# Kernel tuning notes

Hardware: AMD Instinct MI355X
Metric: run time of the kernel (lower is better)

The kernel has to match this reference:

```python
import jax, jax.numpy as jnp
import numpy as np

B, T, A, H, V = 2, 512, 768, 256, 70110  # batch, frames, audio_dim, gru_hidden, vertice_dim


def setup_inputs() -> dict:
    key = jax.random.key(0)
    ks = jax.random.split(key, 16)
    def p(k, shape, s=0.05):
        return jax.random.normal(k, shape, jnp.float32) * s
    return {
        "hidden_states": p(ks[0], (B, T, A), 1.0),
        "template": p(ks[1], (B, V), 1.0),
        "vertice": p(ks[2], (B, T, V), 1.0),
        "tf_mask": jax.random.randint(ks[3], (T,), 0, 2, jnp.int32),
        # GRU layer 0: input 2*A -> H ; layer 1: H -> H (PyTorch gate order r,z,n)
        "w_ih_l0": p(ks[4], (3 * H, 2 * A)),
        "w_hh_l0": p(ks[5], (3 * H, H)),
        "b_ih_l0": p(ks[6], (3 * H,)),
        "b_hh_l0": p(ks[7], (3 * H,)),
        "w_ih_l1": p(ks[8], (3 * H, H)),
        "w_hh_l1": p(ks[9], (3 * H, H)),
        "b_ih_l1": p(ks[10], (3 * H,)),
        "b_hh_l1": p(ks[11], (3 * H,)),
        "fc_w": p(ks[12], (V, H)),
        "fc_b": p(ks[13], (V,)),
        "red_w": p(ks[14], (A, V), 0.005),
        "red_b": p(ks[15], (A,)),
    }


def gru_cell(x, h, w_ih, w_hh, b_ih, b_hh):
    # PyTorch GRUCell math, gates ordered (r, z, n)
    gi = x @ w_ih.T + b_ih
    gh = h @ w_hh.T + b_hh
    i_r, i_z, i_n = jnp.split(gi, 3, axis=-1)
    h_r, h_z, h_n = jnp.split(gh, 3, axis=-1)
    r = jax.nn.sigmoid(i_r + h_r)
    z = jax.nn.sigmoid(i_z + h_z)
    n = jnp.tanh(i_n + r * h_n)
    return (1.0 - z) * n + z * h


def reference(hidden_states, template, vertice, tf_mask,
              w_ih_l0, w_hh_l0, b_ih_l0, b_hh_l0,
              w_ih_l1, w_hh_l1, b_ih_l1, b_hh_l1,
              fc_w, fc_b, red_w, red_b):
    dt = hidden_states.dtype
    cur = template @ red_w.T + red_b            # [B, A] reduced template vertice
    h_l0 = jnp.zeros((B, H), dt)
    h_l1 = jnp.zeros((B, H), dt)

    def step(carry, xs):
        h0, h1, cur = carry
        hs_t, vert_t, tf = xs                   # [B,A], [B,V], scalar int
        x = jnp.concatenate([hs_t, cur], axis=-1)   # [B, 2A]
        h0 = gru_cell(x, h0, w_ih_l0, w_hh_l0, b_ih_l0, b_hh_l0)
        h1 = gru_cell(h0, h1, w_ih_l1, w_hh_l1, b_ih_l1, b_hh_l1)
        pred = h1 @ fc_w.T + fc_b               # [B, V]
        loss_t = jnp.mean((pred - vert_t) ** 2)  # MSE criterion
        # teacher forcing: feed GT frame when tf==1, else own prediction
        src = jnp.where(tf.astype(bool), vert_t, pred)
        cur = src @ red_w.T + red_b             # [B, A]
        return (h0, h1, cur), (pred, loss_t)

    xs = (jnp.swapaxes(hidden_states, 0, 1),    # [T,B,A]
          jnp.swapaxes(vertice, 0, 1),          # [T,B,V]
          tf_mask)                              # [T]
    _, (preds, losses) = jax.lax.scan(step, (h_l0, h_l1, cur), xs)
    vertice_out = jnp.swapaxes(preds, 0, 1)     # [B,T,V]
    loss = jnp.mean(losses)                     # sum_t loss_t / frame_num
    return vertice_out, loss
```

## Files before the change

### kernel.cpp

```cpp
#include <hip/hip_runtime.h>
#include <hip/hip_bf16.h>


#define TT 512
#define VD 70110
#define NR 1024

using bf16x8 = __attribute__((ext_vector_type(8))) short;
using f32x4  = __attribute__((ext_vector_type(4))) float;

static __device__ __forceinline__ unsigned short f2bf(float f) {
  unsigned u = __float_as_uint(f);
  u += 0x7FFFu + ((u >> 16) & 1u);
  return (unsigned short)(u >> 16);
}

__global__ __launch_bounds__(512, 1)
void bigk_merged(const float* __restrict__ A, const float* __restrict__ vert,
                 const float* __restrict__ fcw,
                 float* __restrict__ OUTG, float* __restrict__ OUTM, int CHK)
{
  __shared__ unsigned short Al[256][40];
  __shared__ unsigned short Bl[256][40];
  const int tid = threadIdx.x;
  const bool bform = (blockIdx.x == 4);
  float* C      = bform ? OUTM : OUTG;
  const int ldc = bform ? 256 : 1024;
  const int N   = bform ? 256 : 1024;
  const int n0  = bform ? 0 : blockIdx.x * 256;
  const int m0  = blockIdx.y * 256;
  const int kc0 = blockIdx.z * CHK;
  const int kc1 = min(VD, kc0 + CHK);
  const int wave = tid >> 6, lane = tid & 63;
  const int wm = wave >> 1, wn = wave & 1;
  const int kq = lane >> 4, ln = lane & 15;
  f32x4 acc[4][8] = {};
  for (int kc = kc0; kc < kc1; kc += 32) {
    __syncthreads();
    {
      const int m = tid >> 1, kh = (tid & 1) << 4;
      const float* arow = A + (long)(m0 + m) * (long)VD;
      unsigned short tmp[16] __attribute__((aligned(16)));
      if (kc + 32 <= kc1) {
        const float2* ap2 = (const float2*)(arow + kc + kh);
#pragma unroll
        for (int i = 0; i < 8; ++i) { float2 v = ap2[i]; tmp[2*i] = f2bf(v.x); tmp[2*i+1] = f2bf(v.y); }
      } else {
#pragma unroll
        for (int i = 0; i < 16; ++i) {
          int kk = kc + kh + i;
          tmp[i] = f2bf((kk < kc1) ? arow[kk] : 0.f);
        }
      }
      ((int4*)&Al[m][kh])[0] = *(int4*)&tmp[0];
      ((int4*)&Al[m][kh])[1] = *(int4*)&tmp[8];
    }
    if (!bform) {
      const int n = tid >> 1, kh = (tid & 1) << 4;
      const float* bp = vert + (long)(n0 + n) * (long)VD;
      unsigned short tmp[16] __attribute__((aligned(16)));
      if (kc + 32 <= kc1) {
        const float2* bp2 = (const float2*)(bp + kc + kh);
#pragma unroll
        for (int i = 0; i < 8; ++i) { float2 v = bp2[i]; tmp[2*i] = f2bf(v.x); tmp[2*i+1] = f2bf(v.y); }
      } else {
#pragma unroll
        for (int i = 0; i < 16; ++i) {
          int kk = kc + kh + i;
          tmp[i] = f2bf((kk < kc1) ? bp[kk] : 0.f);
        }
      }
      ((int4*)&Bl[n][kh])[0] = *(int4*)&tmp[0];
      ((int4*)&Bl[n][kh])[1] = *(int4*)&tmp[8];
    } else {
      const int n = tid & 255, kh = (tid >> 8) << 4;
      unsigned short tmp[16] __attribute__((aligned(16)));
#pragma unroll
      for (int i = 0; i < 16; ++i) {
        int kk = kc + kh + i;
        float v = 0.f;
        if (kk < kc1 && n < 256) v = fcw[(long)kk * 256 + n];
        tmp[i] = f2bf(v);
      }
      ((int4*)&Bl[n][kh])[0] = *(int4*)&tmp[0];
      ((int4*)&Bl[n][kh])[1] = *(int4*)&tmp[8];
    }
    __syncthreads();
    bf16x8 af[4], bfv[8];
#pragma unroll
    for (int i = 0; i < 4; ++i) af[i] = *(const bf16x8*)&Al[wm*64 + i*16 + ln][kq*8];
#pragma unroll
    for (int j = 0; j < 8; ++j) bfv[j] = *(const bf16x8*)&Bl[wn*128 + j*16 + ln][kq*8];
#pragma unroll
    for (int i = 0; i < 4; ++i)
#pragma unroll
      for (int j = 0; j < 8; ++j)
        acc[i][j] = __builtin_amdgcn_mfma_f32_16x16x32_bf16(af[i], bfv[j], acc[i][j], 0, 0, 0);
  }
#pragma unroll
  for (int i = 0; i < 4; ++i)
#pragma unroll
    for (int j = 0; j < 8; ++j)
#pragma unroll
      for (int r = 0; r < 4; ++r) {
        int gm = m0 + wm*64 + i*16 + kq*4 + r;
        int gn = n0 + wn*128 + j*16 + ln;
        if (gn < N) unsafeAtomicAdd(&C[(long)gm * ldc + gn], acc[i][j][r]);
      }
}

__global__ __launch_bounds__(256)
void gemv3(const float* __restrict__ redw, const float* __restrict__ tmpl,
           const float* __restrict__ fcb, float* __restrict__ extra)
{
  const int tid = threadIdx.x;
  const int a0 = blockIdx.x * 8;
  const long k0 = (long)blockIdx.y * 8764;
  const long k1 = (k0 + 8764 < (long)VD) ? (k0 + 8764) : (long)VD;
  float s[3][8] = {};
  for (long k = k0 + tid; k < k1; k += 256) {
    const float c0 = tmpl[k], c1 = tmpl[(long)VD + k], cb2 = fcb[k];
#pragma unroll
    for (int r = 0; r < 8; ++r) {
      const float w = redw[(long)(a0 + r) * VD + k];
      s[0][r] += c0 * w; s[1][r] += c1 * w; s[2][r] += cb2 * w;
    }
  }
#pragma unroll
  for (int v = 0; v < 3; ++v)
#pragma unroll
    for (int r = 0; r < 8; ++r) {
      float x = s[v][r];
#pragma unroll
      for (int o = 32; o > 0; o >>= 1) x += __shfl_down(x, o);
      if ((tid & 63) == 0) unsafeAtomicAdd(&extra[v * 768 + a0 + r], x);
    }
}

static __device__ __forceinline__ void transpose_body(
    const float* src, int lds, float* dst, int ldd,
    int rows, int cols, const float* bias, int bx, int by)
{
  __shared__ float tile[32][33];
  const int rb = bx * 32, cb = by * 32;
  const int tx = threadIdx.x & 31, ty = threadIdx.x >> 5;
  for (int yy = ty; yy < 32; yy += 8) {
    int c = cb + yy, r = rb + tx;
    tile[yy][tx] = (c < cols && r < rows) ? src[(long)c * lds + r] : 0.f;
  }
  __syncthreads();
  for (int yy = ty; yy < 32; yy += 8) {
    int r = rb + yy, c = cb + tx;
    if (r < rows && c < cols)
      dst[(long)r * ldd + c] = tile[tx][yy] + (bias ? bias[c] : 0.f);
  }
}

__global__ void transpose_merged(const float* __restrict__ OUTG,
                                 const float* __restrict__ OUTM,
                                 const float* __restrict__ extra,
                                 const float* __restrict__ redb,
                                 float* __restrict__ GF, float* __restrict__ MT)
{
  if (blockIdx.z == 0) {
    transpose_body(OUTG, 1024, GF, 768, 1024, 768, redb, blockIdx.x, blockIdx.y);
  } else {
    if (blockIdx.x < 8) {
      transpose_body(OUTM, 256, MT, 768, 256, 768, nullptr, blockIdx.x, blockIdx.y);
    } else if (blockIdx.x == 8 && blockIdx.y == 0) {
      for (int i = threadIdx.x; i < 3 * 768; i += 256) {
        const int b = i / 768, a = i - b * 768;
        GF[(long)(1024 + b) * 768 + a] = extra[i] + redb[a];
      }
    }
  }
}

__global__ __launch_bounds__(256, 2)
void gemm128x3(const float* __restrict__ hs, const float* __restrict__ wih0,
               float* __restrict__ GIHS, const float* __restrict__ bih0,
               const float* __restrict__ GF, float* __restrict__ PM,
               const float* __restrict__ MT, float* __restrict__ M2)
{
  const float *A, *B, *bias = nullptr; float* C;
  int lda, ldb, M, N, K; long ldc;
  if (blockIdx.z == 0) {
    if (blockIdx.x >= 8) return;
    A = hs; lda = 768; B = wih0; ldb = 1536; C = GIHS; ldc = 768; bias = bih0;
    M = 1024; N = 768; K = 768;
  } else if (blockIdx.z == 1) {
    A = GF; lda = 768; B = wih0 + 768; ldb = 1536; C = PM; ldc = 768;
    M = 1027; N = 768; K = 768;
  } else {
    if (blockIdx.x >= 6 || blockIdx.y >= 2) return;
    A = wih0 + 768; lda = 1536; B = MT; ldb = 768; C = M2; ldc = 256;
    M = 768; N = 256; K = 768;
  }
  __shared__ unsigned short Al[128][40];
  __shared__ unsigned short Bl[128][40];
  const int tid = threadIdx.x;
  const int m0 = blockIdx.x * 128, n0 = blockIdx.y * 128;
  const int wave = tid >> 6, lane = tid & 63;
  const int wm = wave >> 1, wn = wave & 1;
  const int kq = lane >> 4, ln = lane & 15;
  f32x4 acc[4][4] = {};
  for (int kc = 0; kc < K; kc += 32) {
    __syncthreads();
    {
      const int m = tid >> 1, kh = (tid & 1) << 4;
      unsigned short tmp[16] __attribute__((aligned(16)));
      const bool mok = (m0 + m) < M;
      if (mok) {
        const float4* ap4 = (const float4*)(A + (long)(m0 + m) * lda + kc + kh);
#pragma unroll
        for (int i = 0; i < 4; ++i) {
          float4 v = ap4[i];
          tmp[4*i+0] = f2bf(v.x); tmp[4*i+1] = f2bf(v.y);
          tmp[4*i+2] = f2bf(v.z); tmp[4*i+3] = f2bf(v.w);
        }
      } else {
#pragma unroll
        for (int i = 0; i < 16; ++i) tmp[i] = 0;
      }
      ((int4*)&Al[m][kh])[0] = *(int4*)&tmp[0];
      ((int4*)&Al[m][kh])[1] = *(int4*)&tmp[8];
      const int n = m;
      unsigned short tmb[16] __attribute__((aligned(16)));
      const bool nok = (n0 + n) < N;
      if (nok) {
        const float4* bp4 = (const float4*)(B + (long)(n0 + n) * ldb + kc + kh);
#pragma unroll
        for (int i = 0; i < 4; ++i) {
          float4 v = bp4[i];
          tmb[4*i+0] = f2bf(v.x); tmb[4*i+1] = f2bf(v.y);
          tmb[4*i+2] = f2bf(v.z); tmb[4*i+3] = f2bf(v.w);
        }
      } else {
#pragma unroll
        for (int i = 0; i < 16; ++i) tmb[i] = 0;
      }
      ((int4*)&Bl[n][kh])[0] = *(int4*)&tmb[0];
      ((int4*)&Bl[n][kh])[1] = *(int4*)&tmb[8];
    }
    __syncthreads();
    bf16x8 af[4], bfv[4];
#pragma unroll
    for (int i = 0; i < 4; ++i) af[i]  = *(const bf16x8*)&Al[wm*64 + i*16 + ln][kq*8];
#pragma unroll
    for (int j = 0; j < 4; ++j) bfv[j] = *(const bf16x8*)&Bl[wn*64 + j*16 + ln][kq*8];
#pragma unroll
    for (int i = 0; i < 4; ++i)
#pragma unroll
      for (int j = 0; j < 4; ++j)
        acc[i][j] = __builtin_amdgcn_mfma_f32_16x16x32_bf16(af[i], bfv[j], acc[i][j], 0, 0, 0);
  }
#pragma unroll
  for (int i = 0; i < 4; ++i)
#pragma unroll
    for (int j = 0; j < 4; ++j)
#pragma unroll
      for (int r = 0; r < 4; ++r) {
        const int gm = m0 + wm*64 + i*16 + kq*4 + r;
        const int gn = n0 + wn*64 + j*16 + ln;
        if (gm < M && gn < N) {
          float v = acc[i][j][r];
          if (bias) v += bias[gn];
          C[(long)gm * ldc + gn] = v;
        }
      }
}

struct ProdLds {
  float wq[24][260], wh0s[24][260], wi1s[24][260], wh1s[24][260];
  float h0c[2][256], h1c[2][256];
  float dotsS[2][2][3][8];
  int tfl[TT];
};
struct ConsLds {
  unsigned short As[128][264];
  unsigned short Bl[128][40];
  float wred[8];
};

#define HALF_DOTS(W, H, MS)                                                   \
  {                                                                           \
    const int g8_ = tid >> 3, l8_ = tid & 7;                                  \
    if (g8_ < 48) {                                                           \
      const int row_ = g8_ >> 1, bb_ = g8_ & 1;                               \
      const float4* w4_ = (const float4*)&(W)[row_][0];                       \
      const float4* h4_ = (const float4*)&(H)[bb_][0];                        \
      float s_ = 0.f;                                                         \
      _Pragma("unroll")                                                       \
      for (int i = 0; i < 8; ++i) {                                           \
        const float4 a_ = w4_[i * 8 + l8_], h_ = h4_[i * 8 + l8_];            \
        s_ += a_.x * h_.x + a_.y * h_.y + a_.z * h_.z + a_.w * h_.w;          \
      }                                                                       \
      s_ += __shfl_xor(s_, 1); s_ += __shfl_xor(s_, 2); s_ += __shfl_xor(s_, 4); \
      if (l8_ == 0) dotsS[MS][bb_][row_ >> 3][row_ & 7] = s_;                 \
    }                                                                         \
  }

#define POLL_ISSUE(buf, var)                                                  \
  unsigned long long var = __hip_atomic_load(&(buf)[tid], __ATOMIC_RELAXED, __HIP_MEMORY_SCOPE_AGENT);
#define POLL_FINISH(buf, var, dstLds, want)                                   \
  {                                                                           \
    const unsigned w_ = (unsigned)(want); int sp_ = 0;                        \
    while ((unsigned)(var >> 32) < w_ && ++sp_ < (1 << 15)) {                 \
      __builtin_amdgcn_s_sleep(1);                                            \
      var = __hip_atomic_load(&(buf)[tid], __ATOMIC_RELAXED, __HIP_MEMORY_SCOPE_AGENT); \
    }                                                                         \
    ((float*)dstLds)[tid] = __uint_as_float((unsigned)var);                   \
  }
#define POLLP(buf, dstLds, want)                                              \
  { POLL_ISSUE(buf, pw_); POLL_FINISH(buf, pw_, dstLds, want); }

__global__ __launch_bounds__(512, 1)
void k3_fused(const float* __restrict__ gihs, const float* __restrict__ Pm,
              const float* __restrict__ M2m,
              const float* __restrict__ whh0, const float* __restrict__ bhh0,
              const float* __restrict__ wih1, const float* __restrict__ bih1,
              const float* __restrict__ whh1, const float* __restrict__ bhh1,
              const int* __restrict__ tfm,
              unsigned short* __restrict__ h1sb,
              unsigned long long* __restrict__ h0p, unsigned long long* __restrict__ h1p,
              unsigned* __restrict__ prog,
              const float* __restrict__ fcw, const float* __restrict__ fcb,
              const float* __restrict__ vert,
              float* __restrict__ out, float* __restrict__ lossp)
{
  __shared__ union { ProdLds p; ConsLds c; } U;
  const int tid = threadIdx.x;

  if (blockIdx.x >= 32) {
    auto& C = U.c;
    const int idx = blockIdx.x - 32;
    int tx, memb, cnt;
    if (idx < 24)      { tx = 0; memb = (idx)      >> 1; cnt = 12; }
    else if (idx < 48) { tx = 1; memb = (idx - 24) >> 1; cnt = 12; }
    else if (idx < 96) { tx = 2; memb = (idx - 48) >> 1; cnt = 24; }
    else               { tx = 3; memb = (idx - 96) >> 1; cnt = 64; }
    const int b = idx & 1;
    const int nt0 = memb * 548 / cnt, nt1 = (memb + 1) * 548 / cnt;
    if (nt0 >= nt1) return;
    const unsigned want = (unsigned)((tx + 1) * 128);
    if (tid < 32) {
      int sp = 0;
      while (__hip_atomic_load(&prog[tid * 16], __ATOMIC_RELAXED, __HIP_MEMORY_SCOPE_AGENT) < want) {
        if (++sp > (1 << 14)) break;
        for (int j = 0; j < 16; ++j) __builtin_amdgcn_s_sleep(15);
      }
    }
    __syncthreads();
    const long rbase = (long)b * 512 + (long)tx * 128;
    {
      const unsigned long long* src = (const unsigned long long*)(h1sb + rbase * 256);
#pragma unroll
      for (int i = 0; i < 16; ++i) {
        const int u = tid * 16 + i;
        unsigned long long v = __hip_atomic_load(&src[u], __ATOMIC_RELAXED, __HIP_MEMORY_SCOPE_AGENT);
        const int row = u >> 6, c4 = u & 63;
        *(unsigned long long*)&C.As[row][c4 * 4] = v;
      }
    }
    __syncthreads();
    const int wave = tid >> 6, lane = tid & 63;
    const int wm = wave >> 2, wn = wave & 3;
    const int kq = lane >> 4, ln = lane & 15;
    for (int nt = nt0; nt < nt1; ++nt) {
      const int n0 = nt * 128;
      f32x4 acc[4][2] = {};
#pragma unroll 1
      for (int ks = 0; ks < 8; ++ks) {
        __syncthreads();
        {
          const int rn = tid >> 2, kh = (tid & 3) * 8;
          const int gn = n0 + rn;
          unsigned short tmb[8] __attribute__((aligned(16)));
          if (gn < VD) {
            const float4* bp = (const float4*)&fcw[(long)gn * 256 + ks * 32 + kh];
            float4 v0 = bp[0], v1 = bp[1];
            tmb[0] = f2bf(v0.x); tmb[1] = f2bf(v0.y); tmb[2] = f2bf(v0.z); tmb[3] = f2bf(v0.w);
            tmb[4] = f2bf(v1.x); tmb[5] = f2bf(v1.y); tmb[6] = f2bf(v1.z); tmb[7] = f2bf(v1.w);
          } else {
#pragma unroll
            for (int i = 0; i < 8; ++i) tmb[i] = 0;
          }
          *(int4*)&C.Bl[rn][kh] = *(int4*)tmb;
        }
        __syncthreads();
        bf16x8 af[4], bfv[2];
#pragma unroll
        for (int i = 0; i < 4; ++i)
          af[i] = *(const bf16x8*)&C.As[wm*64 + i*16 + ln][ks*32 + kq*8];
#pragma unroll
        for (int j = 0; j < 2; ++j)
          bfv[j] = *(const bf16x8*)&C.Bl[wn*32 + j*16 + ln][kq*8];
#pragma unroll
        for (int i = 0; i < 4; ++i)
#pragma unroll
          for (int j = 0; j < 2; ++j)
            acc[i][j] = __builtin_amdgcn_mfma_f32_16x16x32_bf16(af[i], bfv[j], acc[i][j], 0, 0, 0);
      }
      float ls = 0.f;
#pragma unroll
      for (int i = 0; i < 4; ++i)
#pragma unroll
        for (int j = 0; j < 2; ++j)
#pragma unroll
          for (int r = 0; r < 4; ++r) {
            const int gmL = wm*64 + i*16 + kq*4 + r;
            const int gn = n0 + wn*32 + j*16 + ln;
            if (gn < VD) {
              const float v = acc[i][j][r] + fcb[gn];
              const long grow = rbase + gmL;
              out[grow * VD + gn] = v;
              const float dd = v - vert[grow * VD + gn];
              ls += dd * dd;
            }
          }
#pragma unroll
      for (int o = 32; o > 0; o >>= 1) ls += __shfl_down(ls, o);
      if (lane == 0) C.wred[wave] = ls;
      __syncthreads();
      if (tid == 0) {
        float s = 0.f;
#pragma unroll
        for (int w = 0; w < 8; ++w) s += C.wred[w];
        lossp[(tx * 2 + b) * 548 + nt] = s;
      }
      __syncthreads();
    }
    return;
  }

  float (&wq)[24][260]   = U.p.wq;
  float (&wh0s)[24][260] = U.p.wh0s;
  float (&wi1s)[24][260] = U.p.wi1s;
  float (&wh1s)[24][260] = U.p.wh1s;
  float (&h0c)[2][256]   = U.p.h0c;
  float (&h1c)[2][256]   = U.p.h1c;
  float (&dotsS)[2][2][3][8] = U.p.dotsS;
  int   (&tfl)[TT]       = U.p.tfl;
  const int wg = blockIdx.x;
  const int j0 = wg * 8;

  {
    const int col = tid & 255, rh = tid >> 8;
    for (int row = rh; row < 24; row += 2) {
      const int g = row >> 3, jj = row & 7;
      const long gr = g * 256 + j0 + jj;
      wq[row][col]   = M2m[gr * 256 + col];
      wh0s[row][col] = whh0[gr * 256 + col];
      wi1s[row][col] = wih1[gr * 256 + col];
      wh1s[row][col] = whh1[gr * 256 + col];
    }
  }
  ((float*)h0c)[tid] = 0.f;
  ((float*)h1c)[tid] = 0.f;
  if (tid < TT) tfl[tid] = tfm[tid];

  const int cb = tid >> 3, cjj = tid & 7, cj = j0 + cjj;
  float bh0v[3], bi1v[3], bh1v[3], d2v[3];
  if (tid < 16) {
#pragma unroll
    for (int g = 0; g < 3; ++g) {
      bh0v[g] = bhh0[g*256 + cj];
      bi1v[g] = bih1[g*256 + cj];
      bh1v[g] = bhh1[g*256 + cj];
      d2v[g]  = Pm[(long)1026 * 768 + g*256 + cj];
    }
  }
  __syncthreads();

  const int wave = tid >> 6;
  float gihsv[3], piv[3];
  if (tid < 16) {
#pragma unroll
    for (int g = 0; g < 3; ++g) {
      gihsv[g] = gihs[((long)cb * TT) * 768 + g*256 + cj];
      piv[g]   = Pm[(long)(1024 + cb) * 768 + g*256 + cj];
    }
  }
  for (int t = 0; t < TT; ++t) {
    const int tfprev = (t == 0) ? 1 : tfl[t - 1];
    if (!tfprev) {
      POLL_ISSUE(h1p + (t & 1) * 512, pb);
      HALF_DOTS(wh0s, h0c, 1);
      POLL_FINISH(h1p + (t & 1) * 512, pb, h1c, t);
      __syncthreads();
      HALF_DOTS(wq, h1c, 0);
    } else {
      HALF_DOTS(wh0s, h0c, 1);
    }
    __syncthreads();
    if (tid < 16) {
      float gi[3], gh[3];
#pragma unroll
      for (int g = 0; g < 3; ++g) {
        const float q = tfprev ? 0.f : (dotsS[0][cb][g][cjj] + d2v[g]);
        gi[g] = gihsv[g] + (tfprev ? piv[g] : q);
        gh[g] = dotsS[1][cb][g][cjj] + bh0v[g];
      }
      const float rr = 1.f / (1.f + __expf(-(gi[0] + gh[0])));
      const float zz = 1.f / (1.f + __expf(-(gi[1] + gh[1])));
      const float nn = tanhf(gi[2] + rr * gh[2]);
      const float h0n = (1.f - zz) * nn + zz * h0c[cb][cj];
      const unsigned long long pk =
          ((unsigned long long)(unsigned)(t + 1) << 32) | (unsigned long long)__float_as_uint(h0n);
      __hip_atomic_store(&h0p[((t + 1) & 1) * 512 + cb * 256 + cj], pk,
                         __ATOMIC_RELAXED, __HIP_MEMORY_SCOPE_AGENT);
    }
    if (tid < 16 && t + 1 < TT) {
#pragma unroll
      for (int g = 0; g < 3; ++g) {
        gihsv[g] = gihs[((long)cb * TT + (t + 1)) * 768 + g*256 + cj];
        piv[g]   = Pm[((long)cb * TT + t) * 768 + g*256 + cj];
      }
    }
    __syncthreads();
    POLL_ISSUE(h0p + ((t + 1) & 1) * 512, hw);
    if (tfprev) {
      POLL_ISSUE(h1p + (t & 1) * 512, qb);
      POLL_FINISH(h1p + (t & 1) * 512, qb, h1c, t);
      __syncthreads();
    }
    HALF_DOTS(wh1s, h1c, 1);
    POLL_FINISH(h0p + ((t + 1) & 1) * 512, hw, h0c, t + 1);
    __syncthreads();
    HALF_DOTS(wi1s, h0c, 0);
    __syncthreads();
    if (tid < 16) {
      float gi[3], gh[3];
#pragma unroll
      for (int g = 0; g < 3; ++g) {
        gi[g] = dotsS[0][cb][g][cjj] + bi1v[g];
        gh[g] = dotsS[1][cb][g][cjj] + bh1v[g];
      }
      const float rr = 1.f / (1.f + __expf(-(gi[0] + gh[0])));
      const float zz = 1.f / (1.f + __expf(-(gi[1] + gh[1])));
      const float nn = tanhf(gi[2] + rr * gh[2]);
      const float h1n = (1.f - zz) * nn + zz * h1c[cb][cj];
      const unsigned hb = (unsigned)f2bf(h1n);
      asm volatile("global_store_short %0, %1, off sc0 sc1"
                   :: "v"(&h1sb[((long)cb * TT + t) * 256 + cj]), "v"(hb) : "memory");
      const unsigned long long pk =
          ((unsigned long long)(unsigned)(t + 1) << 32) | (unsigned long long)__float_as_uint(h1n);
      __hip_atomic_store(&h1p[((t + 1) & 1) * 512 + cb * 256 + cj], pk,
                         __ATOMIC_RELAXED, __HIP_MEMORY_SCOPE_AGENT);
    }
    if ((t & 15) == 15) {
      if (wave == 0) asm volatile("s_waitcnt vmcnt(0)" ::: "memory");
      if (tid == 0)
        __hip_atomic_store(&prog[wg * 16], (unsigned)(t + 1),
                           __ATOMIC_RELAXED, __HIP_MEMORY_SCOPE_AGENT);
    }
    __syncthreads();
  }
}

__global__ void loss_finalize(const float* __restrict__ lossp, int n, float* __restrict__ out) {
  __shared__ float red[256];
  float s = 0.f;
  for (int i = threadIdx.x; i < n; i += 256) s += lossp[i];
  red[threadIdx.x] = s;
  __syncthreads();
  for (int st = 128; st > 0; st >>= 1) {
    if (threadIdx.x < st) red[threadIdx.x] += red[threadIdx.x + st];
    __syncthreads();
  }
  if (threadIdx.x == 0) out[0] = red[0] * (1.0f / 71792640.0f);
}

extern "C" void kernel_launch(void* const* d_in, const int* in_sizes, int n_in,
                              void* d_out, int out_size, void* d_ws, size_t ws_size,
                              hipStream_t stream) {
  (void)in_sizes; (void)n_in; (void)out_size; (void)ws_size;
  const float* hs   = (const float*)d_in[0];
  const float* tmpl = (const float*)d_in[1];
  const float* vert = (const float*)d_in[2];
  const int*   tfm  = (const int*)  d_in[3];
  const float* wih0 = (const float*)d_in[4];
  const float* whh0 = (const float*)d_in[5];
  const float* bih0 = (const float*)d_in[6];
  const float* bhh0 = (const float*)d_in[7];
  const float* wih1 = (const float*)d_in[8];
  const float* whh1 = (const float*)d_in[9];
  const float* bih1 = (const float*)d_in[10];
  const float* bhh1 = (const float*)d_in[11];
  const float* fcw  = (const float*)d_in[12];
  const float* fcb  = (const float*)d_in[13];
  const float* redw = (const float*)d_in[14];
  const float* redb = (const float*)d_in[15];
  float* out = (float*)d_out;

  char* ws = (char*)d_ws;
  float*    LOSSP = (float*)(ws + 0);
  float*    OUTG  = (float*)(ws + 0);
  float*    OUTM  = (float*)(ws + 3145728);
  float*    EXTRA = (float*)(ws + 3932160);
  unsigned long long* H0P = (unsigned long long*)(ws + 3941376);
  unsigned long long* H1P = (unsigned long long*)(ws + 3949568);
  unsigned* PROG  = (unsigned*)(ws + 3957760);
  float*    GF    = (float*)(ws + 3960064);
  float*    MT    = (float*)(ws + 7115776);
  float*    GIHS  = (float*)(ws + 7902208);
  float*    PM    = (float*)(ws + 11047936);
  float*    M2    = (float*)(ws + 14203648);
  unsigned short* H1SB = (unsigned short*)(ws + 14990080);

  hipMemsetAsync(d_ws, 0, 3960064, stream);

  bigk_merged<<<dim3(5, 3, 21), 512, 0, stream>>>(redw, vert, fcw, OUTG, OUTM, 3344);
  gemv3<<<dim3(96, 8), 256, 0, stream>>>(redw, tmpl, fcb, EXTRA);

  transpose_merged<<<dim3(32, 24, 2), 256, 0, stream>>>(OUTG, OUTM, EXTRA, redb, GF, MT);

  gemm128x3<<<dim3(9, 6, 3), 256, 0, stream>>>(hs, wih0, GIHS, bih0, GF, PM, MT, M2);

  k3_fused<<<256, 512, 0, stream>>>(GIHS, PM, M2, whh0, bhh0, wih1, bih1, whh1, bhh1,
                                    tfm, H1SB, H0P, H1P, PROG,
                                    fcw, fcb, vert, out, LOSSP);

  loss_finalize<<<1, 256, 0, stream>>>(LOSSP, 4384, out + 71792640L);
}
```

Baseline: 2.891 ms.

## Skew GRU layers so teacher-forced steps need one cross-workgroup sync

Restructures the recurrent producer loop so layer-0 step t+1 is computed alongside layer-1 step t. In teacher-forced steps all three matvec halves run together, and both hidden-state exchanges are polled in a single phase instead of two serialized grid-wide waits. Non-teacher-forced steps keep two phases, because the reduced prediction feedback needs h1 first. It adds a peeled first and last step, separate thread groups for the two layers' gate math, and more LDS dot slots. The risk is in correctness of the step-tagged ping-pong buffers and the POLLP helper.

```diff
diff --git a/kernel.cpp b/kernel.cpp
--- a/kernel.cpp
+++ b/kernel.cpp
@@ -273,7 +273,7 @@
 struct ProdLds {
   float wq[24][260], wh0s[24][260], wi1s[24][260], wh1s[24][260];
   float h0c[2][256], h1c[2][256];
-  float dotsS[2][2][3][8];
+  float dotsS[4][2][3][8];
   int tfl[TT];
 };
 struct ConsLds {
@@ -281,6 +281,11 @@
   unsigned short Bl[128][40];
   float wred[8];
 };
+
+#define S_Q  0
+#define S_GH 1
+#define S_I1 2
+#define S_H1 3
 
 #define HALF_DOTS(W, H, MS)                                                   \
   {                                                                           \
@@ -439,7 +444,7 @@
   float (&wh1s)[24][260] = U.p.wh1s;
   float (&h0c)[2][256]   = U.p.h0c;
   float (&h1c)[2][256]   = U.p.h1c;
-  float (&dotsS)[2][2][3][8] = U.p.dotsS;
+  float (&dotsS)[4][2][3][8] = U.p.dotsS;
   int   (&tfl)[TT]       = U.p.tfl;
   const int wg = blockIdx.x;
   const int j0 = wg * 8;
@@ -459,15 +464,19 @@
   ((float*)h1c)[tid] = 0.f;
   if (tid < TT) tfl[tid] = tfm[tid];
 
-  const int cb = tid >> 3, cjj = tid & 7, cj = j0 + cjj;
+  const int cb = (tid >> 3) & 1, cjj = tid & 7, cj = j0 + cjj;
   float bh0v[3], bi1v[3], bh1v[3], d2v[3];
   if (tid < 16) {
 #pragma unroll
     for (int g = 0; g < 3; ++g) {
       bh0v[g] = bhh0[g*256 + cj];
+      d2v[g]  = Pm[(long)1026 * 768 + g*256 + cj];
+    }
+  } else if (tid < 32) {
+#pragma unroll
+    for (int g = 0; g < 3; ++g) {
       bi1v[g] = bih1[g*256 + cj];
       bh1v[g] = bhh1[g*256 + cj];
-      d2v[g]  = Pm[(long)1026 * 768 + g*256 + cj];
     }
   }
   __syncthreads();
@@ -481,60 +490,164 @@
       piv[g]   = Pm[(long)(1024 + cb) * 768 + g*256 + cj];
     }
   }
-  for (int t = 0; t < TT; ++t) {
-    const int tfprev = (t == 0) ? 1 : tfl[t - 1];
-    if (!tfprev) {
-      POLL_ISSUE(h1p + (t & 1) * 512, pb);
-      HALF_DOTS(wh0s, h0c, 1);
-      POLL_FINISH(h1p + (t & 1) * 512, pb, h1c, t);
-      __syncthreads();
-      HALF_DOTS(wq, h1c, 0);
+  HALF_DOTS(wh0s, h0c, S_GH);
+  __syncthreads();
+  if (tid < 16) {
+    float gi[3], gh[3];
+#pragma unroll
+    for (int g = 0; g < 3; ++g) {
+      gi[g] = gihsv[g] + piv[g];
+      gh[g] = dotsS[S_GH][cb][g][cjj] + bh0v[g];
+    }
+    const float rr = 1.f / (1.f + __expf(-(gi[0] + gh[0])));
+    const float zz = 1.f / (1.f + __expf(-(gi[1] + gh[1])));
+    const float nn = tanhf(gi[2] + rr * gh[2]);
+    const float h0n = (1.f - zz) * nn;
+    const unsigned long long pk =
+        ((unsigned long long)1u << 32) | (unsigned long long)__float_as_uint(h0n);
+    __hip_atomic_store(&h0p[512 + cb * 256 + cj], pk,
+                       __ATOMIC_RELAXED, __HIP_MEMORY_SCOPE_AGENT);
+#pragma unroll
+    for (int g = 0; g < 3; ++g) {
+      gihsv[g] = gihs[((long)cb * TT + 1) * 768 + g*256 + cj];
+      piv[g]   = Pm[((long)cb * TT + 0) * 768 + g*256 + cj];
+    }
+  }
+  __syncthreads();
+  POLLP(h0p + 512, h0c, 1);
+  __syncthreads();
+
+  for (int t = 0; t < TT - 1; ++t) {
+    const int tfc = tfl[t];
+    if (tfc) {
+      HALF_DOTS(wh0s, h0c, S_GH);
+      HALF_DOTS(wi1s, h0c, S_I1);
+      HALF_DOTS(wh1s, h1c, S_H1);
+      __syncthreads();
+      if (tid < 16) {
+        float gi[3], gh[3];
+#pragma unroll
+        for (int g = 0; g < 3; ++g) {
+          gi[g] = gihsv[g] + piv[g];
+          gh[g] = dotsS[S_GH][cb][g][cjj] + bh0v[g];
+        }
+        const float rr = 1.f / (1.f + __expf(-(gi[0] + gh[0])));
+        const float zz = 1.f / (1.f + __expf(-(gi[1] + gh[1])));
+        const float nn = tanhf(gi[2] + rr * gh[2]);
+        const float h0n = (1.f - zz) * nn + zz * h0c[cb][cj];
+        const unsigned long long pk =
+            ((unsigned long long)(unsigned)(t + 2) << 32) | (unsigned long long)__float_as_uint(h0n);
+        __hip_atomic_store(&h0p[(t & 1) * 512 + cb * 256 + cj], pk,
+                           __ATOMIC_RELAXED, __HIP_MEMORY_SCOPE_AGENT);
+        if (t + 1 < TT - 1) {
+#pragma unroll
+          for (int g = 0; g < 3; ++g) {
+            gihsv[g] = gihs[((long)cb * TT + (t + 2)) * 768 + g*256 + cj];
+            piv[g]   = Pm[((long)cb * TT + (t + 1)) * 768 + g*256 + cj];
+          }
+        }
+      } else if (tid < 32) {
+        float gi[3], gh[3];
+#pragma unroll
+        for (int g = 0; g < 3; ++g) {
+          gi[g] = dotsS[S_I1][cb][g][cjj] + bi1v[g];
+          gh[g] = dotsS[S_H1][cb][g][cjj] + bh1v[g];
+        }
+        const float rr = 1.f / (1.f + __expf(-(gi[0] + gh[0])));
+        const float zz = 1.f / (1.f + __expf(-(gi[1] + gh[1])));
+        const float nn = tanhf(gi[2] + rr * gh[2]);
+        const float h1n = (1.f - zz) * nn + zz * h1c[cb][cj];
+        const unsigned hb = (unsigned)f2bf(h1n);
+        asm volatile("global_store_short %0, %1, off sc0 sc1"
+                     :: "v"(&h1sb[((long)cb * TT + t) * 256 + cj]), "v"(hb) : "memory");
+        const unsigned long long pk =
+            ((unsigned long long)(unsigned)(t + 1) << 32) | (unsigned long long)__float_as_uint(h1n);
+        __hip_atomic_store(&h1p[((t + 1) & 1) * 512 + cb * 256 + cj], pk,
+                           __ATOMIC_RELAXED, __HIP_MEMORY_SCOPE_AGENT);
+      }
+      __syncthreads();
+      POLL_ISSUE(h0p + (t & 1) * 512, pa);
+      POLL_ISSUE(h1p + ((t + 1) & 1) * 512, pb);
+      POLL_FINISH(h0p + (t & 1) * 512, pa, h0c, t + 2);
+      POLL_FINISH(h1p + ((t + 1) & 1) * 512, pb, h1c, t + 1);
+      __syncthreads();
     } else {
-      HALF_DOTS(wh0s, h0c, 1);
-    }
-    __syncthreads();
-    if (tid < 16) {
+      HALF_DOTS(wi1s, h0c, S_I1);
+      HALF_DOTS(wh1s, h1c, S_H1);
+      __syncthreads();
+      if (tid >= 16 && tid < 32) {
+        float gi[3], gh[3];
+#pragma unroll
+        for (int g = 0; g < 3; ++g) {
+          gi[g] = dotsS[S_I1][cb][g][cjj] + bi1v[g];
+          gh[g] = dotsS[S_H1][cb][g][cjj] + bh1v[g];
+        }
+        const float rr = 1.f / (1.f + __expf(-(gi[0] + gh[0])));
+        const float zz = 1.f / (1.f + __expf(-(gi[1] + gh[1])));
+        const float nn = tanhf(gi[2] + rr * gh[2]);
+        const float h1n = (1.f - zz) * nn + zz * h1c[cb][cj];
+        const unsigned hb = (unsigned)f2bf(h1n);
+        asm volatile("global_store_short %0, %1, off sc0 sc1"
+                     :: "v"(&h1sb[((long)cb * TT + t) * 256 + cj]), "v"(hb) : "memory");
+        const unsigned long long pk =
+            ((unsigned long long)(unsigned)(t + 1) << 32) | (unsigned long long)__float_as_uint(h1n);
+        __hip_atomic_store(&h1p[((t + 1) & 1) * 512 + cb * 256 + cj], pk,
+                           __ATOMIC_RELAXED, __HIP_MEMORY_SCOPE_AGENT);
+      }
+      __syncthreads();
+      POLL_ISSUE(h1p + ((t + 1) & 1) * 512, pq);
+      HALF_DOTS(wh0s, h0c, S_GH);
+      POLL_FINISH(h1p + ((t + 1) & 1) * 512, pq, h1c, t + 1);
+      __syncthreads();
+      HALF_DOTS(wq, h1c, S_Q);
+      __syncthreads();
+      if (tid < 16) {
+        float gi[3], gh[3];
+#pragma unroll
+        for (int g = 0; g < 3; ++g) {
+          const float q = dotsS[S_Q][cb][g][cjj] + d2v[g];
+          gi[g] = gihsv[g] + q;
+          gh[g] = dotsS[S_GH][cb][g][cjj] + bh0v[g];
+        }
+        const float rr = 1.f / (1.f + __expf(-(gi[0] + gh[0])));
+        const float zz = 1.f / (1.f + __expf(-(gi[1] + gh[1])));
+        const float nn = tanhf(gi[2] + rr * gh[2]);
+        const float h0n = (1.f - zz) * nn + zz * h0c[cb][cj];
+        const unsigned long long pk =
+            ((unsigned long long)(unsigned)(t + 2) << 32) | (unsigned long long)__float_as_uint(h0n);
+        __hip_atomic_store(&h0p[(t & 1) * 512 + cb * 256 + cj], pk,
+                           __ATOMIC_RELAXED, __HIP_MEMORY_SCOPE_AGENT);
+        if (t + 1 < TT - 1) {
+#pragma unroll
+          for (int g = 0; g < 3; ++g) {
+            gihsv[g] = gihs[((long)cb * TT + (t + 2)) * 768 + g*256 + cj];
+            piv[g]   = Pm[((long)cb * TT + (t + 1)) * 768 + g*256 + cj];
+          }
+        }
+      }
+      __syncthreads();
+      POLLP(h0p + (t & 1) * 512, h0c, t + 2);
+      __syncthreads();
+    }
+    if ((t & 15) == 15) {
+      if (wave == 0) asm volatile("s_waitcnt vmcnt(0)" ::: "memory");
+      if (tid == 0)
+        __hip_atomic_store(&prog[wg * 16], (unsigned)(t + 1),
+                           __ATOMIC_RELAXED, __HIP_MEMORY_SCOPE_AGENT);
+    }
+    __syncthreads();
+  }
+  {
+    const int t = TT - 1;
+    HALF_DOTS(wi1s, h0c, S_I1);
+    HALF_DOTS(wh1s, h1c, S_H1);
+    __syncthreads();
+    if (tid >= 16 && tid < 32) {
       float gi[3], gh[3];
 #pragma unroll
       for (int g = 0; g < 3; ++g) {
-        const float q = tfprev ? 0.f : (dotsS[0][cb][g][cjj] + d2v[g]);
-        gi[g] = gihsv[g] + (tfprev ? piv[g] : q);
-        gh[g] = dotsS[1][cb][g][cjj] + bh0v[g];
-      }
-      const float rr = 1.f / (1.f + __expf(-(gi[0] + gh[0])));
-      const float zz = 1.f / (1.f + __expf(-(gi[1] + gh[1])));
-      const float nn = tanhf(gi[2] + rr * gh[2]);
-      const float h0n = (1.f - zz) * nn + zz * h0c[cb][cj];
-      const unsigned long long pk =
-          ((unsigned long long)(unsigned)(t + 1) << 32) | (unsigned long long)__float_as_uint(h0n);
-      __hip_atomic_store(&h0p[((t + 1) & 1) * 512 + cb * 256 + cj], pk,
-                         __ATOMIC_RELAXED, __HIP_MEMORY_SCOPE_AGENT);
-    }
-    if (tid < 16 && t + 1 < TT) {
-#pragma unroll
-      for (int g = 0; g < 3; ++g) {
-        gihsv[g] = gihs[((long)cb * TT + (t + 1)) * 768 + g*256 + cj];
-        piv[g]   = Pm[((long)cb * TT + t) * 768 + g*256 + cj];
-      }
-    }
-    __syncthreads();
-    POLL_ISSUE(h0p + ((t + 1) & 1) * 512, hw);
-    if (tfprev) {
-      POLL_ISSUE(h1p + (t & 1) * 512, qb);
-      POLL_FINISH(h1p + (t & 1) * 512, qb, h1c, t);
-      __syncthreads();
-    }
-    HALF_DOTS(wh1s, h1c, 1);
-    POLL_FINISH(h0p + ((t + 1) & 1) * 512, hw, h0c, t + 1);
-    __syncthreads();
-    HALF_DOTS(wi1s, h0c, 0);
-    __syncthreads();
-    if (tid < 16) {
-      float gi[3], gh[3];
-#pragma unroll
-      for (int g = 0; g < 3; ++g) {
-        gi[g] = dotsS[0][cb][g][cjj] + bi1v[g];
-        gh[g] = dotsS[1][cb][g][cjj] + bh1v[g];
+        gi[g] = dotsS[S_I1][cb][g][cjj] + bi1v[g];
+        gh[g] = dotsS[S_H1][cb][g][cjj] + bh1v[g];
       }
       const float rr = 1.f / (1.f + __expf(-(gi[0] + gh[0])));
       const float zz = 1.f / (1.f + __expf(-(gi[1] + gh[1])));
@@ -543,18 +656,11 @@
       const unsigned hb = (unsigned)f2bf(h1n);
       asm volatile("global_store_short %0, %1, off sc0 sc1"
                    :: "v"(&h1sb[((long)cb * TT + t) * 256 + cj]), "v"(hb) : "memory");
-      const unsigned long long pk =
-          ((unsigned long long)(unsigned)(t + 1) << 32) | (unsigned long long)__float_as_uint(h1n);
-      __hip_atomic_store(&h1p[((t + 1) & 1) * 512 + cb * 256 + cj], pk,
+    }
+    if (wave == 0) asm volatile("s_waitcnt vmcnt(0)" ::: "memory");
+    if (tid == 0)
+      __hip_atomic_store(&prog[wg * 16], (unsigned)TT,
                          __ATOMIC_RELAXED, __HIP_MEMORY_SCOPE_AGENT);
-    }
-    if ((t & 15) == 15) {
-      if (wave == 0) asm volatile("s_waitcnt vmcnt(0)" ::: "memory");
-      if (tid == 0)
-        __hip_atomic_store(&prog[wg * 16], (unsigned)(t + 1),
-                           __ATOMIC_RELAXED, __HIP_MEMORY_SCOPE_AGENT);
-    }
-    __syncthreads();
   }
 }
 
```

New measurement: 2.937 ms. No clear change (+1.6%).

## Pre-convert big operands to padded bf16 and use direct-to-LDS loads in big GEMM

Applied to the files above, without the earlier changes.

Adds a tobf16 pass that converts red_w, vertice and fc_w once to bf16. The K dimension of red_w and vertice is padded to a multiple of 32. A new bigk_bf16 kernel streams these with global_load_lds into unpadded LDS tiles, and the fused recurrent kernel reads fc_w from the bf16 copy instead of converting fp32 on the fly. This halves the bytes read by the GEMMs and removes conversion work from their inner loops. In exchange it adds extra conversion passes that read all the fp32 data once, needs about 300MB of workspace (with a fallback to the old path if that is missing), and removes the LDS padding that likely avoided bank conflicts.

```diff
diff --git a/kernel.cpp b/kernel.cpp
--- a/kernel.cpp
+++ b/kernel.cpp
@@ -4,6 +4,7 @@
 
 #define TT 512
 #define VD 70110
+#define VDP 70144
 #define NR 1024
 
 using bf16x8 = __attribute__((ext_vector_type(8))) short;
@@ -13,6 +14,107 @@
   unsigned u = __float_as_uint(f);
   u += 0x7FFFu + ((u >> 16) & 1u);
   return (unsigned short)(u >> 16);
+}
+
+__global__ __launch_bounds__(256)
+void tobf16(const float* __restrict__ src, unsigned short* __restrict__ dst,
+            long srcStride, long dstStride, int colsSrc, int colsDst)
+{
+  const long row = blockIdx.y;
+  const int c0 = (blockIdx.x * 256 + threadIdx.x) * 8;
+  if (c0 >= colsDst) return;
+  const float* s = src + row * srcStride;
+  unsigned short* d = dst + row * dstStride;
+  if (c0 + 8 <= colsSrc) {
+    const float2* s2 = (const float2*)(s + c0);
+    unsigned short t[8] __attribute__((aligned(16)));
+#pragma unroll
+    for (int i = 0; i < 4; ++i) { float2 v = s2[i]; t[2*i] = f2bf(v.x); t[2*i+1] = f2bf(v.y); }
+    *(int4*)(d + c0) = *(int4*)t;
+  } else {
+#pragma unroll
+    for (int i = 0; i < 8; ++i) {
+      int c = c0 + i;
+      if (c < colsDst) d[c] = (c < colsSrc) ? f2bf(s[c]) : (unsigned short)0;
+    }
+  }
+}
+
+__global__ __launch_bounds__(512, 1)
+void bigk_bf16(const unsigned short* __restrict__ RB,
+               const unsigned short* __restrict__ VB,
+               const unsigned short* __restrict__ FB,
+               float* __restrict__ OUTG, float* __restrict__ OUTM, int CHK)
+{
+  __shared__ unsigned short Al[256][32];
+  __shared__ unsigned short Bl[256][32];
+  const int tid = threadIdx.x;
+  const bool bform = (blockIdx.x == 4);
+  float* C      = bform ? OUTM : OUTG;
+  const int ldc = bform ? 256 : 1024;
+  const int n0  = bform ? 0 : blockIdx.x * 256;
+  const int m0  = blockIdx.y * 256;
+  const int kc0 = blockIdx.z * CHK;
+  const int kc1 = min(VDP, kc0 + CHK);
+  const int wave = tid >> 6, lane = tid & 63;
+  const int wm = wave >> 1, wn = wave & 1;
+  const int kq = lane >> 4, ln = lane & 15;
+  const int rowL = tid >> 2, segL = tid & 3;
+  f32x4 acc[4][8] = {};
+  for (int kc = kc0; kc < kc1; kc += 32) {
+    __syncthreads();
+    {
+      void* ldsA = (void*)((char*)&Al[0][0] + (tid >> 6) * 1024);
+#pragma unroll
+      for (int iss = 0; iss < 2; ++iss) {
+        const int gL = iss * 512 + tid;
+        const int row = gL >> 2, seg = gL & 3;
+        const unsigned short* src = RB + (long)(m0 + row) * VDP + kc + seg * 8;
+        __builtin_amdgcn_global_load_lds((const void*)src,
+                                         (void*)((char*)ldsA + iss * 8192), 16, 0, 0);
+      }
+      (void)rowL; (void)segL;
+    }
+    if (!bform) {
+      void* ldsB = (void*)((char*)&Bl[0][0] + (tid >> 6) * 1024);
+#pragma unroll
+      for (int iss = 0; iss < 2; ++iss) {
+        const int gL = iss * 512 + tid;
+        const int row = gL >> 2, seg = gL & 3;
+        const unsigned short* src = VB + (long)(n0 + row) * VDP + kc + seg * 8;
+        __builtin_amdgcn_global_load_lds((const void*)src,
+                                         (void*)((char*)ldsB + iss * 8192), 16, 0, 0);
+      }
+    } else {
+      const int n = tid & 255, kh = (tid >> 8) << 4;
+#pragma unroll
+      for (int i = 0; i < 16; ++i) {
+        const int kk = kc + kh + i;
+        Bl[n][kh + i] = (kk < VD) ? FB[(long)kk * 256 + n] : (unsigned short)0;
+      }
+    }
+    __syncthreads();
+    bf16x8 af[4], bfv[8];
+#pragma unroll
+    for (int i = 0; i < 4; ++i) af[i] = *(const bf16x8*)&Al[wm*64 + i*16 + ln][kq*8];
+#pragma unroll
+    for (int j = 0; j < 8; ++j) bfv[j] = *(const bf16x8*)&Bl[wn*128 + j*16 + ln][kq*8];
+#pragma unroll
+    for (int i = 0; i < 4; ++i)
+#pragma unroll
+      for (int j = 0; j < 8; ++j)
+        acc[i][j] = __builtin_amdgcn_mfma_f32_16x16x32_bf16(af[i], bfv[j], acc[i][j], 0, 0, 0);
+  }
+#pragma unroll
+  for (int i = 0; i < 4; ++i)
+#pragma unroll
+    for (int j = 0; j < 8; ++j)
+#pragma unroll
+      for (int r = 0; r < 4; ++r) {
+        const int gm = m0 + wm*64 + i*16 + kq*4 + r;
+        const int gn = n0 + wn*128 + j*16 + ln;
+        unsafeAtomicAdd(&C[(long)gm * ldc + gn], acc[i][j][r]);
+      }
 }
 
 __global__ __launch_bounds__(512, 1)
@@ -324,8 +426,9 @@
               unsigned short* __restrict__ h1sb,
               unsigned long long* __restrict__ h0p, unsigned long long* __restrict__ h1p,
               unsigned* __restrict__ prog,
-              const float* __restrict__ fcw, const float* __restrict__ fcb,
-              const float* __restrict__ vert,
+              const float* __restrict__ fcw, const unsigned short* __restrict__ FB,
+              int useFB,
+              const float* __restrict__ fcb, const float* __restrict__ vert,
               float* __restrict__ out, float* __restrict__ lossp)
 {
   __shared__ union { ProdLds p; ConsLds c; } U;
@@ -375,17 +478,23 @@
         {
           const int rn = tid >> 2, kh = (tid & 3) * 8;
           const int gn = n0 + rn;
-          unsigned short tmb[8] __attribute__((aligned(16)));
-          if (gn < VD) {
-            const float4* bp = (const float4*)&fcw[(long)gn * 256 + ks * 32 + kh];
-            float4 v0 = bp[0], v1 = bp[1];
-            tmb[0] = f2bf(v0.x); tmb[1] = f2bf(v0.y); tmb[2] = f2bf(v0.z); tmb[3] = f2bf(v0.w);
-            tmb[4] = f2bf(v1.x); tmb[5] = f2bf(v1.y); tmb[6] = f2bf(v1.z); tmb[7] = f2bf(v1.w);
+          if (useFB) {
+            int4 v = {0, 0, 0, 0};
+            if (gn < VD) v = *(const int4*)(FB + (long)gn * 256 + ks * 32 + kh);
+            *(int4*)&C.Bl[rn][kh] = v;
           } else {
-#pragma unroll
-            for (int i = 0; i < 8; ++i) tmb[i] = 0;
+            unsigned short tmb[8] __attribute__((aligned(16)));
+            if (gn < VD) {
+              const float4* bp = (const float4*)&fcw[(long)gn * 256 + ks * 32 + kh];
+              float4 v0 = bp[0], v1 = bp[1];
+              tmb[0] = f2bf(v0.x); tmb[1] = f2bf(v0.y); tmb[2] = f2bf(v0.z); tmb[3] = f2bf(v0.w);
+              tmb[4] = f2bf(v1.x); tmb[5] = f2bf(v1.y); tmb[6] = f2bf(v1.z); tmb[7] = f2bf(v1.w);
+            } else {
+#pragma unroll
+              for (int i = 0; i < 8; ++i) tmb[i] = 0;
+            }
+            *(int4*)&C.Bl[rn][kh] = *(int4*)tmb;
           }
-          *(int4*)&C.Bl[rn][kh] = *(int4*)tmb;
         }
         __syncthreads();
         bf16x8 af[4], bfv[2];
@@ -574,7 +683,7 @@
 extern "C" void kernel_launch(void* const* d_in, const int* in_sizes, int n_in,
                               void* d_out, int out_size, void* d_ws, size_t ws_size,
                               hipStream_t stream) {
-  (void)in_sizes; (void)n_in; (void)out_size; (void)ws_size;
+  (void)in_sizes; (void)n_in; (void)out_size;
   const float* hs   = (const float*)d_in[0];
   const float* tmpl = (const float*)d_in[1];
   const float* vert = (const float*)d_in[2];
@@ -607,10 +716,22 @@
   float*    PM    = (float*)(ws + 11047936);
   float*    M2    = (float*)(ws + 14203648);
   unsigned short* H1SB = (unsigned short*)(ws + 14990080);
+  unsigned short* RB = (unsigned short*)(ws + 15514624);
+  unsigned short* VB = (unsigned short*)(ws + 123255808);
+  unsigned short* FB = (unsigned short*)(ws + 266910720);
+  const size_t NEEDED = 302807040UL;
+  const int useBF = (ws_size >= NEEDED) ? 1 : 0;
 
   hipMemsetAsync(d_ws, 0, 3960064, stream);
 
-  bigk_merged<<<dim3(5, 3, 21), 512, 0, stream>>>(redw, vert, fcw, OUTG, OUTM, 3344);
+  if (useBF) {
+    tobf16<<<dim3(35, 768),  256, 0, stream>>>(redw, RB, VD, VDP, VD, VDP);
+    tobf16<<<dim3(35, 1024), 256, 0, stream>>>(vert, VB, VD, VDP, VD, VDP);
+    tobf16<<<dim3(8764, 1),  256, 0, stream>>>(fcw,  FB, 17948160L, 17948160L, 17948160, 17948160);
+    bigk_bf16<<<dim3(5, 3, 17), 512, 0, stream>>>(RB, VB, FB, OUTG, OUTM, 4128);
+  } else {
+    bigk_merged<<<dim3(5, 3, 21), 512, 0, stream>>>(redw, vert, fcw, OUTG, OUTM, 3344);
+  }
   gemv3<<<dim3(96, 8), 256, 0, stream>>>(redw, tmpl, fcb, EXTRA);
 
   transpose_merged<<<dim3(32, 24, 2), 256, 0, stream>>>(OUTG, OUTM, EXTRA, redb, GF, MT);
@@ -619,7 +740,7 @@
 
   k3_fused<<<256, 512, 0, stream>>>(GIHS, PM, M2, whh0, bhh0, wih1, bih1, whh1, bhh1,
                                     tfm, H1SB, H0P, H1P, PROG,
-                                    fcw, fcb, vert, out, LOSSP);
+                                    fcw, FB, useBF, fcb, vert, out, LOSSP);
 
   loss_finalize<<<1, 256, 0, stream>>>(LOSSP, 4384, out + 71792640L);
 }
```

New measurement: 3.135 ms. 1.08x slower.
